# Optimization experiments

Hardware: AMD Instinct MI355X
Metric: run time of the kernel (lower is better)

The kernel has to match this reference:

```python
import jax, jax.numpy as jnp
import numpy as np


def _sum_matrix():
    # [69, 42] mask matrix reproducing compute_sums exactly (incl. bugs):
    # feature k = sum over cells where M[k] == 1, board flattened row-major (6x7).
    M = np.zeros((69, 42), dtype=np.float32)
    m = M.reshape(69, 6, 7)
    # 24 row window sums
    for row in range(6):
        for i in range(4):
            m[row * 4 + i, row, i:i + 4] = 1.0
    # 21 column window sums
    for col in range(7):
        for i in range(3):
            m[24 + col * 3 + i, i:i + 4, col] = 1.0
    # 12 'upward diag' sums: source sums the FULL 4x4 block of the row-flipped
    # board, i.e. original rows (2-off)..(5-off), cols col..col+3.
    for off in range(3):
        for col in range(4):
            m[45 + off * 4 + col, 2 - off:6 - off, col:col + 4] = 1.0
    # 12 'downward diag' sums: allocated but never written in source -> zeros.
    return jnp.asarray(M)


_M = _sum_matrix()  # [69, 42]


def setup_inputs() -> dict:
    key = jax.random.key(0)
    k1, k2, k3 = jax.random.split(key, 3)
    B = 524288
    game_state = jax.random.normal(k1, (B, 42), dtype=jnp.float32)
    W = jax.random.normal(k2, (7, 111), dtype=jnp.float32) * (1.0 / np.sqrt(111.0))
    b = jax.random.normal(k3, (7,), dtype=jnp.float32) * 0.01
    return {"game_state": game_state, "W": W, "b": b}


def reference(game_state, W, b):
    # sums: [B, 69] = all windowed sums as one GEMM against the mask matrix
    sums = game_state @ _M.T
    feats = jnp.concatenate([game_state, sums], axis=1)  # [B, 111]
    return feats @ W.T + b  # [B, 7]
```

## Files before the change

### kernel.cpp

```cpp
#include <hip/hip_runtime.h>


#define ROW_PAD 43

__global__ __launch_bounds__(256)
void ddqn_fused(const float* __restrict__ gs,
                const float* __restrict__ W,
                const float* __restrict__ b,
                float* __restrict__ out) {
    __shared__ float wl[7 * 44];
    __shared__ float bl[7];
    __shared__ float tile[4][64 * ROW_PAD];
    __shared__ float obuf[4][64 * 7];

    const int t = threadIdx.x;
    const int w = t >> 6;
    const int l = t & 63;
    float* tw = tile[w];

    const size_t tileIdx = (size_t)blockIdx.x * 4 + w;
    const float* src = gs + tileIdx * (64 * 42);

    {
        int row = l / 42;
        int col = l - row * 42;
        #pragma unroll
        for (int k = 0; k < 42; ++k) {
            tw[row * ROW_PAD + col] = src[k * 64 + l];
            row += 1; col += 22;
            if (col >= 42) { col -= 42; row += 1; }
        }
    }

    for (int i = t; i < 7 * 44; i += 256) {
        int j = i / 44, d = i - j * 44;
        float acc = 0.0f;
        if (d < 42) {
            acc = W[j * 111 + d];
            int r = d / 7, c = d - r * 7;
            const float* ws = W + j * 111 + 42;
            #pragma unroll
            for (int i4 = 0; i4 < 4; ++i4)
                if (c >= i4 && c <= i4 + 3) acc += ws[r * 4 + i4];
            #pragma unroll
            for (int i3 = 0; i3 < 3; ++i3)
                if (r >= i3 && r <= i3 + 3) acc += ws[24 + c * 3 + i3];
            #pragma unroll
            for (int off = 0; off < 3; ++off)
                #pragma unroll
                for (int col4 = 0; col4 < 4; ++col4)
                    if (r >= 2 - off && r <= 5 - off && c >= col4 && c <= col4 + 3)
                        acc += ws[45 + off * 4 + col4];
        }
        wl[i] = acc;
    }
    if (t < 7) bl[t] = b[t];
    __syncthreads();

    float acc[7];
    #pragma unroll
    for (int j = 0; j < 7; ++j) acc[j] = bl[j];

    const float* xrow = tw + l * ROW_PAD;
    const float4* wl4 = (const float4*)wl;
    #pragma unroll
    for (int dq = 0; dq < 44; dq += 4) {
        float x0 = xrow[dq];
        float x1 = xrow[dq + 1];
        float x2 = (dq + 2 < 42) ? xrow[dq + 2] : 0.0f;
        float x3 = (dq + 3 < 42) ? xrow[dq + 3] : 0.0f;
        #pragma unroll
        for (int j = 0; j < 7; ++j) {
            const float4 wv = wl4[j * 11 + (dq >> 2)];
            acc[j] = fmaf(x0, wv.x, acc[j]);
            acc[j] = fmaf(x1, wv.y, acc[j]);
            acc[j] = fmaf(x2, wv.z, acc[j]);
            acc[j] = fmaf(x3, wv.w, acc[j]);
        }
    }

    float* ob = obuf[w];
    #pragma unroll
    for (int j = 0; j < 7; ++j) ob[l * 7 + j] = acc[j];
    __builtin_amdgcn_wave_barrier();
    float* o = out + tileIdx * 448;
    #pragma unroll
    for (int k = 0; k < 7; ++k) o[k * 64 + l] = ob[k * 64 + l];
}

extern "C" void kernel_launch(void* const* d_in, const int* in_sizes, int n_in,
                              void* d_out, int out_size, void* d_ws, size_t ws_size,
                              hipStream_t stream) {
    const float* gs = (const float*)d_in[0];
    const float* W  = (const float*)d_in[1];
    const float* b  = (const float*)d_in[2];
    float* out = (float*)d_out;

    int B = in_sizes[0] / 42;
    int tiles = B / 64;
    ddqn_fused<<<dim3(tiles / 4), dim3(256), 0, stream>>>(gs, W, b, out);
}
```

Baseline: 151.3 us.

## Load input tiles directly into LDS with global_load_lds and drop output staging

Replaces the per-element register-staged transposed copy of each 64-row tile into padded LDS with direct global-to-LDS DMA loads (16-byte chunks plus a 4-byte tail) into an unpadded layout. Each thread then reads its 42-element row into registers before the FMA loop. The shared output buffer is removed, so each thread writes its 7 outputs straight to global memory, and bias is read from global. This cuts VGPR traffic and LDS usage, but unpadded rows of 42 floats may cause LDS bank conflicts, and the output stores are strided per thread rather than coalesced.

```diff
diff --git a/kernel.cpp b/kernel.cpp
--- a/kernel.cpp
+++ b/kernel.cpp
@@ -1,17 +1,15 @@
 #include <hip/hip_runtime.h>
 
 
-#define ROW_PAD 43
+#define TILE_F 2688
 
 __global__ __launch_bounds__(256)
 void ddqn_fused(const float* __restrict__ gs,
                 const float* __restrict__ W,
                 const float* __restrict__ b,
                 float* __restrict__ out) {
-    __shared__ float wl[7 * 44];
-    __shared__ float bl[7];
-    __shared__ float tile[4][64 * ROW_PAD];
-    __shared__ float obuf[4][64 * 7];
+    __shared__ __align__(16) float wl[7 * 44];
+    __shared__ __align__(16) float tile[4][TILE_F];
 
     const int t = threadIdx.x;
     const int w = t >> 6;
@@ -19,17 +17,21 @@
     float* tw = tile[w];
 
     const size_t tileIdx = (size_t)blockIdx.x * 4 + w;
-    const float* src = gs + tileIdx * (64 * 42);
+    const float* src = gs + tileIdx * TILE_F;
 
-    {
-        int row = l / 42;
-        int col = l - row * 42;
-        #pragma unroll
-        for (int k = 0; k < 42; ++k) {
-            tw[row * ROW_PAD + col] = src[k * 64 + l];
-            row += 1; col += 22;
-            if (col >= 42) { col -= 42; row += 1; }
-        }
+    #pragma unroll
+    for (int k = 0; k < 10; ++k) {
+        __builtin_amdgcn_global_load_lds(
+            (const __attribute__((address_space(1))) void*)(src + k * 256 + l * 4),
+            (__attribute__((address_space(3))) void*)(tw + k * 256),
+            16, 0, 0);
+    }
+    #pragma unroll
+    for (int m = 0; m < 2; ++m) {
+        __builtin_amdgcn_global_load_lds(
+            (const __attribute__((address_space(1))) void*)(src + 2560 + m * 64 + l),
+            (__attribute__((address_space(3))) void*)(tw + 2560 + m * 64),
+            4, 0, 0);
     }
 
     for (int i = t; i < 7 * 44; i += 256) {
@@ -48,44 +50,40 @@
             #pragma unroll
             for (int off = 0; off < 3; ++off)
                 #pragma unroll
-                for (int col4 = 0; col4 < 4; ++col4)
-                    if (r >= 2 - off && r <= 5 - off && c >= col4 && c <= col4 + 3)
-                        acc += ws[45 + off * 4 + col4];
+                for (int c4 = 0; c4 < 4; ++c4)
+                    if (r >= 2 - off && r <= 5 - off && c >= c4 && c <= c4 + 3)
+                        acc += ws[45 + off * 4 + c4];
         }
         wl[i] = acc;
     }
-    if (t < 7) bl[t] = b[t];
     __syncthreads();
+
+    float x[44];
+    const float* xr = tw + l * 42;
+    #pragma unroll
+    for (int d = 0; d < 42; ++d) x[d] = xr[d];
+    x[42] = x[43] = 0.0f;
 
     float acc[7];
     #pragma unroll
-    for (int j = 0; j < 7; ++j) acc[j] = bl[j];
+    for (int j = 0; j < 7; ++j) acc[j] = b[j];
 
-    const float* xrow = tw + l * ROW_PAD;
     const float4* wl4 = (const float4*)wl;
     #pragma unroll
-    for (int dq = 0; dq < 44; dq += 4) {
-        float x0 = xrow[dq];
-        float x1 = xrow[dq + 1];
-        float x2 = (dq + 2 < 42) ? xrow[dq + 2] : 0.0f;
-        float x3 = (dq + 3 < 42) ? xrow[dq + 3] : 0.0f;
+    for (int dq = 0; dq < 11; ++dq) {
         #pragma unroll
         for (int j = 0; j < 7; ++j) {
-            const float4 wv = wl4[j * 11 + (dq >> 2)];
-            acc[j] = fmaf(x0, wv.x, acc[j]);
-            acc[j] = fmaf(x1, wv.y, acc[j]);
-            acc[j] = fmaf(x2, wv.z, acc[j]);
-            acc[j] = fmaf(x3, wv.w, acc[j]);
+            const float4 wv = wl4[j * 11 + dq];
+            acc[j] = fmaf(x[dq * 4 + 0], wv.x, acc[j]);
+            acc[j] = fmaf(x[dq * 4 + 1], wv.y, acc[j]);
+            acc[j] = fmaf(x[dq * 4 + 2], wv.z, acc[j]);
+            acc[j] = fmaf(x[dq * 4 + 3], wv.w, acc[j]);
         }
     }
 
-    float* ob = obuf[w];
+    float* o = out + (tileIdx * 64 + l) * 7;
     #pragma unroll
-    for (int j = 0; j < 7; ++j) ob[l * 7 + j] = acc[j];
-    __builtin_amdgcn_wave_barrier();
-    float* o = out + tileIdx * 448;
-    #pragma unroll
-    for (int k = 0; k < 7; ++k) o[k * 64 + l] = ob[k * 64 + l];
+    for (int j = 0; j < 7; ++j) o[j] = acc[j];
 }
 
 extern "C" void kernel_launch(void* const* d_in, const int* in_sizes, int n_in,
```

Measured after the change: 149.5 us. About the same (-1.2%).
